# Performance work log

Hardware: AMD Instinct MI355X
Metric: run time of the kernel (lower is better)

The kernel has to match this reference:

```python
import jax, jax.numpy as jnp
import numpy as np

B, M, H = 8, 2048, 1024


def setup_inputs() -> dict:
    key = jax.random.key(0)
    k0, k1, k2, k3, k4 = jax.random.split(key, 5)
    return {
        "query": jax.random.normal(k0, (B, M, H), dtype=jnp.float32),
        "key": jax.random.normal(k1, (B, M, H), dtype=jnp.float32),
        "span": jax.random.uniform(k2, (B, M, 2), dtype=jnp.float32),
        "value": jax.random.normal(k3, (B, M, H), dtype=jnp.float32),
        "key_pe": jax.random.normal(k4, (1, H, M), dtype=jnp.float32),
    }


def reference(query, key, span, value, key_pe):
    # Faithful to the source's returned value:
    #   attn_cont (span-gathered version) is overwritten by the dense q @ k^T,
    #   and the scaled/softmaxed `attn` (content + positional) is computed but
    #   NEVER used for the output. The module returns attn_cont @ value with
    #   no scaling and no softmax. span / key_pe do not affect the output.
    attn_cont = jnp.einsum('bmh,bnh->bmn', query, key)  # [B, M, M]
    out = jnp.matmul(attn_cont, value)                   # [B, M, H]
    return out
```

## Files before the change

kernel.cpp:

```cpp
#include <hip/hip_runtime.h>
#include <hip/hip_bf16.h>

typedef __attribute__((ext_vector_type(4))) float f32x4;
typedef __attribute__((ext_vector_type(8))) short bf16x8;
typedef unsigned short u16;


__device__ __forceinline__ u16 f2bf(float f) {
  union { float f; unsigned int u; } v;
  v.f = f;
  unsigned int r = (v.u + 0x7fffu + ((v.u >> 16) & 1u)) >> 16;
  return (u16)r;
}

__device__ __forceinline__ void async16(const void* g, const void* l) {
  __builtin_amdgcn_global_load_lds(
      (const __attribute__((address_space(1))) unsigned int*)(unsigned long)g,
      (__attribute__((address_space(3))) unsigned int*)(unsigned int)(unsigned long)l,
      16, 0, 0);
}


__global__ __launch_bounds__(256) void cvt_plain(const float* __restrict__ in,
                                                 u16* __restrict__ out, int n4) {
  int stride = gridDim.x * blockDim.x;
  for (int i = blockIdx.x * blockDim.x + threadIdx.x; i < n4; i += stride) {
    f32x4 v = *(const f32x4*)(in + (long)i * 4);
    ushort4 o;
    o.x = f2bf(v.x); o.y = f2bf(v.y); o.z = f2bf(v.z); o.w = f2bf(v.w);
    *(ushort4*)(out + (long)i * 4) = o;
  }
}


__global__ __launch_bounds__(256) void cvt_transpose(const float* __restrict__ in,
                                                     u16* __restrict__ out,
                                                     int R, int C) {
  __shared__ u16 tile[64][68];
  const long bo = (long)blockIdx.z * (long)R * (long)C;
  const int r0 = blockIdx.y * 64;
  const int c0 = blockIdx.x * 64;
  const int t = threadIdx.x;
  const int tr = t >> 4;
  const int tc4 = (t & 15) * 4;

#pragma unroll
  for (int i = 0; i < 4; ++i) {
    int r = i * 16 + tr;
    f32x4 v = *(const f32x4*)(in + bo + (long)(r0 + r) * C + c0 + tc4);
    tile[tc4 + 0][r] = f2bf(v.x);
    tile[tc4 + 1][r] = f2bf(v.y);
    tile[tc4 + 2][r] = f2bf(v.z);
    tile[tc4 + 3][r] = f2bf(v.w);
  }
  __syncthreads();
#pragma unroll
  for (int i = 0; i < 4; ++i) {
    int c = i * 16 + tr;
    ushort4 u = *(const ushort4*)(&tile[c][tc4]);
    *(ushort4*)(out + bo + (long)(c0 + c) * R + r0 + tc4) = u;
  }
}


#define BM 128
#define BN 128
#define BK 32

template <bool BF16OUT>
__global__ __launch_bounds__(256, 3) void gemm_nt(const u16* __restrict__ A,
                                                  const u16* __restrict__ Bt,
                                                  void* __restrict__ Cv,
                                                  int M, int N, int K,
                                                  long sA, long sB, long sC) {
  __shared__ u16 As[2][BM][BK];
  __shared__ u16 Bs[2][BN][BK];

  const int b = blockIdx.z;
  A  += (long)b * sA;
  Bt += (long)b * sB;

  const int bn0 = blockIdx.x * BN;
  const int bm0 = blockIdx.y * BM;

  const int tid  = threadIdx.x;
  const int lane = tid & 63;
  const int wave = tid >> 6;
  const int wr = wave >> 1;
  const int wc = wave & 1;
  const int l16 = lane & 15;
  const int kh  = lane >> 4;

  const u16* Abase = A + (long)bm0 * K;
  const u16* Bbase = Bt + (long)bn0 * K;

  const int u0 = wave * 64 + lane;

  f32x4 acc[4][4] = {};

  const int NT = K / BK;
  int cur = 0;

#pragma unroll
  for (int i = 0; i < 2; ++i) {
    int u = i * 256 + u0;
    async16(Abase + (long)(u >> 2) * K + (u & 3) * 8,
            (const char*)(&As[0][0][0]) + i * 4096 + wave * 1024);
    async16(Bbase + (long)(u >> 2) * K + (u & 3) * 8,
            (const char*)(&Bs[0][0][0]) + i * 4096 + wave * 1024);
  }
  asm volatile("s_waitcnt vmcnt(0)" ::: "memory");
  __syncthreads();

  for (int t = 0; t < NT; ++t) {
    if (t + 1 < NT) {
      const int k0 = (t + 1) * BK;
      const int nb = cur ^ 1;
#pragma unroll
      for (int i = 0; i < 2; ++i) {
        int u = i * 256 + u0;
        async16(Abase + k0 + (long)(u >> 2) * K + (u & 3) * 8,
                (const char*)(&As[nb][0][0]) + i * 4096 + wave * 1024);
        async16(Bbase + k0 + (long)(u >> 2) * K + (u & 3) * 8,
                (const char*)(&Bs[nb][0][0]) + i * 4096 + wave * 1024);
      }
    }

    bf16x8 af[4], bfr[4];
#pragma unroll
    for (int i = 0; i < 4; ++i) {
      af[i]  = *(const bf16x8*)(&As[cur][wr * 64 + i * 16 + l16][kh * 8]);
      bfr[i] = *(const bf16x8*)(&Bs[cur][wc * 64 + i * 16 + l16][kh * 8]);
    }
#pragma unroll
    for (int i = 0; i < 4; ++i)
#pragma unroll
      for (int j = 0; j < 4; ++j)
        acc[i][j] =
            __builtin_amdgcn_mfma_f32_16x16x32_bf16(af[i], bfr[j], acc[i][j], 0, 0, 0);

    asm volatile("s_waitcnt vmcnt(0)" ::: "memory");
    __syncthreads();
    cur ^= 1;
  }

  u16*   Cb = (u16*)Cv + (long)b * sC;
  float* Cf = (float*)Cv + (long)b * sC;
#pragma unroll
  for (int i = 0; i < 4; ++i) {
    const int gm = bm0 + wr * 64 + i * 16 + kh * 4;
#pragma unroll
    for (int j = 0; j < 4; ++j) {
      const int gn = bn0 + wc * 64 + j * 16 + l16;
#pragma unroll
      for (int r = 0; r < 4; ++r) {
        if (BF16OUT)
          Cb[(long)(gm + r) * N + gn] = f2bf(acc[i][j][r]);
        else
          Cf[(long)(gm + r) * N + gn] = acc[i][j][r];
      }
    }
  }
}


extern "C" void kernel_launch(void* const* d_in, const int* in_sizes, int n_in,
                              void* d_out, int out_size, void* d_ws, size_t ws_size,
                              hipStream_t stream) {
  const float* Q  = (const float*)d_in[0];
  const float* Kf = (const float*)d_in[1];
  const float* V  = (const float*)d_in[3];
  float* out = (float*)d_out;

  const int B = 8, M = 2048, H = 1024;
  const size_t bmh2 = (size_t)B * M * H * 2;

  char* ws = (char*)d_ws;
  u16* Qb = (u16*)(ws);
  u16* Kt = (u16*)(ws + bmh2);
  u16* Vt = (u16*)(ws + 2 * bmh2);
  u16* Pt = (u16*)(ws + 3 * bmh2);

  cvt_plain<<<2048, 256, 0, stream>>>(Q, Qb, B * M * H / 4);
  cvt_transpose<<<dim3(H / 64, M / 64, B), 256, 0, stream>>>(Kf, Kt, M, H);
  cvt_transpose<<<dim3(H / 64, M / 64, B), 256, 0, stream>>>(V, Vt, M, H);

  gemm_nt<true><<<dim3(H / BN, H / BM, B), 256, 0, stream>>>(
      Vt, Kt, (void*)Pt, H, H, M, (long)H * M, (long)H * M, (long)H * H);

  gemm_nt<false><<<dim3(H / BN, M / BM, B), 256, 0, stream>>>(
      Qb, Pt, (void*)out, M, H, H, (long)M * H, (long)H * H, (long)M * H);
}
```

Baseline: 162.0 us.

## Restructure GEMM to 256x128 tiles, BK64 with XOR-swizzled LDS, fuse K/V conversion

The GEMM kernel moves from 128x128x32 tiles with 256 threads to 256x128x64 tiles with 512 threads. LDS is XOR-swizzled to avoid bank conflicts, and the next stage's global-to-LDS load is issued after the fragment reads. The kernel also uses s_setprio around the MFMA blocks and a flattened grid with batch-interleaved block mapping. The K and V transpose-conversions are merged into a single launch. The aim is more data reuse per tile, fewer LDS conflicts and fewer launches, at the cost of higher register and LDS pressure and sizes now hardcoded.

```diff
diff --git a/kernel.cpp b/kernel.cpp
--- a/kernel.cpp
+++ b/kernel.cpp
@@ -4,6 +4,7 @@
 typedef __attribute__((ext_vector_type(4))) float f32x4;
 typedef __attribute__((ext_vector_type(8))) short bf16x8;
 typedef unsigned short u16;
+typedef unsigned int u32;
 
 
 __device__ __forceinline__ u16 f2bf(float f) {
@@ -19,6 +20,14 @@
       (__attribute__((address_space(3))) unsigned int*)(unsigned int)(unsigned long)l,
       16, 0, 0);
 }
+
+__device__ __forceinline__ void bar() {
+  asm volatile("" ::: "memory");
+  __builtin_amdgcn_s_barrier();
+  asm volatile("" ::: "memory");
+}
+
+#define WAIT_VM0() asm volatile("s_waitcnt vmcnt(0)" ::: "memory")
 
 
 __global__ __launch_bounds__(256) void cvt_plain(const float* __restrict__ in,
@@ -33,11 +42,16 @@
 }
 
 
-__global__ __launch_bounds__(256) void cvt_transpose(const float* __restrict__ in,
-                                                     u16* __restrict__ out,
-                                                     int R, int C) {
+__global__ __launch_bounds__(256) void cvt_kv(const float* __restrict__ Kin,
+                                              const float* __restrict__ Vin,
+                                              u16* __restrict__ Kt,
+                                              u16* __restrict__ Vt) {
   __shared__ u16 tile[64][68];
-  const long bo = (long)blockIdx.z * (long)R * (long)C;
+  const int z = blockIdx.z;
+  const int bsel = z >> 1;
+  const float* in = (z & 1) ? Kin : Vin;
+  u16* out = (z & 1) ? Kt : Vt;
+  const long bo = (long)bsel * 2048 * 1024;
   const int r0 = blockIdx.y * 64;
   const int c0 = blockIdx.x * 64;
   const int t = threadIdx.x;
@@ -47,7 +61,7 @@
 #pragma unroll
   for (int i = 0; i < 4; ++i) {
     int r = i * 16 + tr;
-    f32x4 v = *(const f32x4*)(in + bo + (long)(r0 + r) * C + c0 + tc4);
+    f32x4 v = *(const f32x4*)(in + bo + (long)(r0 + r) * 1024 + c0 + tc4);
     tile[tc4 + 0][r] = f2bf(v.x);
     tile[tc4 + 1][r] = f2bf(v.y);
     tile[tc4 + 2][r] = f2bf(v.z);
@@ -58,106 +72,157 @@
   for (int i = 0; i < 4; ++i) {
     int c = i * 16 + tr;
     ushort4 u = *(const ushort4*)(&tile[c][tc4]);
-    *(ushort4*)(out + bo + (long)(c0 + c) * R + r0 + tc4) = u;
-  }
-}
-
-
-#define BM 128
-#define BN 128
-#define BK 32
+    *(ushort4*)(out + bo + (long)(c0 + c) * 2048 + r0 + tc4) = u;
+  }
+}
 
 template <bool BF16OUT>
-__global__ __launch_bounds__(256, 3) void gemm_nt(const u16* __restrict__ A,
+__global__ __launch_bounds__(512, 2) void gemm_nt(const u16* __restrict__ A,
                                                   const u16* __restrict__ Bt,
                                                   void* __restrict__ Cv,
-                                                  int M, int N, int K,
+                                                  int K, int NT, int nTN,
                                                   long sA, long sB, long sC) {
-  __shared__ u16 As[2][BM][BK];
-  __shared__ u16 Bs[2][BN][BK];
-
-  const int b = blockIdx.z;
-  A  += (long)b * sA;
-  Bt += (long)b * sB;
-
-  const int bn0 = blockIdx.x * BN;
-  const int bm0 = blockIdx.y * BM;
-
-  const int tid  = threadIdx.x;
+  __shared__ u16 As[2][256][64];
+  __shared__ u16 Bs[2][128][64];
+
+  const int bid = blockIdx.x;
+  const int b = bid & 7;
+  const int tile = bid >> 3;
+  const int bn0 = (tile % nTN) * 128;
+  const int bm0 = (tile / nTN) * 256;
+
+  const int tid = threadIdx.x;
   const int lane = tid & 63;
   const int wave = tid >> 6;
-  const int wr = wave >> 1;
-  const int wc = wave & 1;
+  const int wr = wave >> 2;
+  const int wc = wave & 3;
   const int l16 = lane & 15;
-  const int kh  = lane >> 4;
-
-  const u16* Abase = A + (long)bm0 * K;
-  const u16* Bbase = Bt + (long)bn0 * K;
-
-  const int u0 = wave * 64 + lane;
-
-  f32x4 acc[4][4] = {};
-
-  const int NT = K / BK;
-  int cur = 0;
-
+  const int kh = lane >> 4;
+
+  const char* Ab = (const char*)(A + (long)b * sA);
+  const char* Bb = (const char*)(Bt + (long)b * sB);
+
+  const int rowbytes = K * 2;
+  int aoff[4], boff[2];
+#pragma unroll
+  for (int i = 0; i < 4; ++i) {
+    int u = tid + i * 512;
+    int row = u >> 3, sl = (u & 7) ^ (row & 7);
+    aoff[i] = (bm0 + row) * rowbytes + sl * 16;
+  }
 #pragma unroll
   for (int i = 0; i < 2; ++i) {
-    int u = i * 256 + u0;
-    async16(Abase + (long)(u >> 2) * K + (u & 3) * 8,
-            (const char*)(&As[0][0][0]) + i * 4096 + wave * 1024);
-    async16(Bbase + (long)(u >> 2) * K + (u & 3) * 8,
-            (const char*)(&Bs[0][0][0]) + i * 4096 + wave * 1024);
-  }
-  asm volatile("s_waitcnt vmcnt(0)" ::: "memory");
-  __syncthreads();
+    int u = tid + i * 512;
+    int row = u >> 3, sl = (u & 7) ^ (row & 7);
+    boff[i] = (bn0 + row) * rowbytes + sl * 16;
+  }
+
+#define STG_A(buf)                                                          \
+  {                                                                         \
+    _Pragma("unroll") for (int i_ = 0; i_ < 4; ++i_) {                      \
+      async16(Ab + aoff[i_], (char*)&As[buf][0][0] + (tid + i_ * 512) * 16);\
+      aoff[i_] += 128;                                                      \
+    }                                                                       \
+  }
+#define STG_B(buf)                                                          \
+  {                                                                         \
+    _Pragma("unroll") for (int i_ = 0; i_ < 2; ++i_) {                      \
+      async16(Bb + boff[i_], (char*)&Bs[buf][0][0] + (tid + i_ * 512) * 16);\
+      boff[i_] += 128;                                                      \
+    }                                                                       \
+  }
+
+  int offA[2][4][2];
+#pragma unroll
+  for (int q = 0; q < 2; ++q)
+#pragma unroll
+    for (int f = 0; f < 4; ++f) {
+      int r = q * 128 + wr * 64 + f * 16 + l16;
+#pragma unroll
+      for (int ks = 0; ks < 2; ++ks)
+        offA[q][f][ks] = r * 64 + (((ks * 4 + kh) ^ (l16 & 7)) * 8);
+    }
+  int offB[2][2];
+#pragma unroll
+  for (int fn = 0; fn < 2; ++fn) {
+    int r = fn * 64 + wc * 16 + l16;
+#pragma unroll
+    for (int ks = 0; ks < 2; ++ks)
+      offB[fn][ks] = r * 64 + (((ks * 4 + kh) ^ (l16 & 7)) * 8);
+  }
+
+  f32x4 acc[8][2] = {};
+  bf16x8 ar[4][2], br[2][2];
+
+  STG_A(0); STG_B(0);
+  WAIT_VM0();
+  bar();
 
   for (int t = 0; t < NT; ++t) {
-    if (t + 1 < NT) {
-      const int k0 = (t + 1) * BK;
-      const int nb = cur ^ 1;
-#pragma unroll
-      for (int i = 0; i < 2; ++i) {
-        int u = i * 256 + u0;
-        async16(Abase + k0 + (long)(u >> 2) * K + (u & 3) * 8,
-                (const char*)(&As[nb][0][0]) + i * 4096 + wave * 1024);
-        async16(Bbase + k0 + (long)(u >> 2) * K + (u & 3) * 8,
-                (const char*)(&Bs[nb][0][0]) + i * 4096 + wave * 1024);
-      }
-    }
-
-    bf16x8 af[4], bfr[4];
-#pragma unroll
-    for (int i = 0; i < 4; ++i) {
-      af[i]  = *(const bf16x8*)(&As[cur][wr * 64 + i * 16 + l16][kh * 8]);
-      bfr[i] = *(const bf16x8*)(&Bs[cur][wc * 64 + i * 16 + l16][kh * 8]);
-    }
-#pragma unroll
-    for (int i = 0; i < 4; ++i)
-#pragma unroll
-      for (int j = 0; j < 4; ++j)
-        acc[i][j] =
-            __builtin_amdgcn_mfma_f32_16x16x32_bf16(af[i], bfr[j], acc[i][j], 0, 0, 0);
-
-    asm volatile("s_waitcnt vmcnt(0)" ::: "memory");
-    __syncthreads();
-    cur ^= 1;
-  }
+    const int cur = t & 1, nxt = cur ^ 1;
+    const bool g = (t + 1 < NT);
+    const u16* Abuf = &As[cur][0][0];
+    const u16* Bbuf = &Bs[cur][0][0];
+
+#pragma unroll
+    for (int f = 0; f < 4; ++f)
+#pragma unroll
+      for (int ks = 0; ks < 2; ++ks)
+        ar[f][ks] = *(const bf16x8*)(Abuf + offA[0][f][ks]);
+#pragma unroll
+    for (int fn = 0; fn < 2; ++fn)
+#pragma unroll
+      for (int ks = 0; ks < 2; ++ks)
+        br[fn][ks] = *(const bf16x8*)(Bbuf + offB[fn][ks]);
+
+    if (g) { STG_A(nxt); STG_B(nxt); }
+
+    __builtin_amdgcn_s_setprio(1);
+#pragma unroll
+    for (int f = 0; f < 4; ++f)
+#pragma unroll
+      for (int n = 0; n < 2; ++n)
+#pragma unroll
+        for (int ks = 0; ks < 2; ++ks)
+          acc[f][n] = __builtin_amdgcn_mfma_f32_16x16x32_bf16(
+              ar[f][ks], br[n][ks], acc[f][n], 0, 0, 0);
+    __builtin_amdgcn_s_setprio(0);
+
+#pragma unroll
+    for (int f = 0; f < 4; ++f)
+#pragma unroll
+      for (int ks = 0; ks < 2; ++ks)
+        ar[f][ks] = *(const bf16x8*)(Abuf + offA[1][f][ks]);
+
+    __builtin_amdgcn_s_setprio(1);
+#pragma unroll
+    for (int f = 0; f < 4; ++f)
+#pragma unroll
+      for (int n = 0; n < 2; ++n)
+#pragma unroll
+        for (int ks = 0; ks < 2; ++ks)
+          acc[4 + f][n] = __builtin_amdgcn_mfma_f32_16x16x32_bf16(
+              ar[f][ks], br[n][ks], acc[4 + f][n], 0, 0, 0);
+    __builtin_amdgcn_s_setprio(0);
+
+    if (g) WAIT_VM0();
+    bar();
+  }
+#undef STG_A
+#undef STG_B
 
   u16*   Cb = (u16*)Cv + (long)b * sC;
   float* Cf = (float*)Cv + (long)b * sC;
 #pragma unroll
-  for (int i = 0; i < 4; ++i) {
-    const int gm = bm0 + wr * 64 + i * 16 + kh * 4;
-#pragma unroll
-    for (int j = 0; j < 4; ++j) {
-      const int gn = bn0 + wc * 64 + j * 16 + l16;
+  for (int fm = 0; fm < 8; ++fm) {
+    const int gm = bm0 + (fm >> 2) * 128 + wr * 64 + (fm & 3) * 16 + kh * 4;
+#pragma unroll
+    for (int fn = 0; fn < 2; ++fn) {
+      const int gn = bn0 + fn * 64 + wc * 16 + l16;
 #pragma unroll
       for (int r = 0; r < 4; ++r) {
-        if (BF16OUT)
-          Cb[(long)(gm + r) * N + gn] = f2bf(acc[i][j][r]);
-        else
-          Cf[(long)(gm + r) * N + gn] = acc[i][j][r];
+        if (BF16OUT) Cb[(long)(gm + r) * 1024 + gn] = f2bf(acc[fm][fn][r]);
+        else         Cf[(long)(gm + r) * 1024 + gn] = acc[fm][fn][r];
       }
     }
   }
@@ -172,22 +237,20 @@
   const float* V  = (const float*)d_in[3];
   float* out = (float*)d_out;
 
-  const int B = 8, M = 2048, H = 1024;
-  const size_t bmh2 = (size_t)B * M * H * 2;
-
   char* ws = (char*)d_ws;
-  u16* Qb = (u16*)(ws);
-  u16* Kt = (u16*)(ws + bmh2);
-  u16* Vt = (u16*)(ws + 2 * bmh2);
-  u16* Pt = (u16*)(ws + 3 * bmh2);
-
-  cvt_plain<<<2048, 256, 0, stream>>>(Q, Qb, B * M * H / 4);
-  cvt_transpose<<<dim3(H / 64, M / 64, B), 256, 0, stream>>>(Kf, Kt, M, H);
-  cvt_transpose<<<dim3(H / 64, M / 64, B), 256, 0, stream>>>(V, Vt, M, H);
-
-  gemm_nt<true><<<dim3(H / BN, H / BM, B), 256, 0, stream>>>(
-      Vt, Kt, (void*)Pt, H, H, M, (long)H * M, (long)H * M, (long)H * H);
-
-  gemm_nt<false><<<dim3(H / BN, M / BM, B), 256, 0, stream>>>(
-      Qb, Pt, (void*)out, M, H, H, (long)M * H, (long)H * H, (long)M * H);
-}
+  u16* Vt = (u16*)(ws);
+  u16* Kt = (u16*)(ws + (size_t)32 * 1024 * 1024);
+  u16* Pt = (u16*)(ws + (size_t)64 * 1024 * 1024);
+  u16* Qb = (u16*)(ws + (size_t)80 * 1024 * 1024);
+
+  cvt_kv<<<dim3(16, 32, 16), 256, 0, stream>>>(Kf, V, Kt, Vt);
+  cvt_plain<<<4096, 256, 0, stream>>>(Q, Qb, 8 * 2048 * 1024 / 4);
+
+  gemm_nt<true><<<256, 512, 0, stream>>>(
+      Vt, Kt, (void*)Pt, 2048, 32, 8,
+      (long)1024 * 2048, (long)1024 * 2048, (long)1024 * 1024);
+
+  gemm_nt<false><<<512, 512, 0, stream>>>(
+      Qb, Pt, (void*)out, 1024, 16, 8,
+      (long)2048 * 1024, (long)1024 * 1024, (long)2048 * 1024);
+}
```

Result: faster. 136.0 us (-16.0%).
